# Performance work log

Hardware: AMD Instinct MI355X
Metric: run time of the kernel (lower is better)

The kernel has to match this reference:

```python
import jax, jax.numpy as jnp
import numpy as np

B, C, H, W = 4, 256, 64, 64
HID = C // 2


def setup_inputs() -> dict:
    key = jax.random.key(0)
    kx, kp, kt, kg, km = jax.random.split(key, 5)
    return {
        "x": jax.random.normal(kx, (B, C, H, W), dtype=jnp.float32),
        "w_phi": jax.random.normal(kp, (HID, C), dtype=jnp.float32) * 0.02,
        "w_theta": jax.random.normal(kt, (HID, C), dtype=jnp.float32) * 0.02,
        "w_g": jax.random.normal(kg, (HID, C), dtype=jnp.float32) * 0.02,
        "w_mask": jax.random.normal(km, (C, HID), dtype=jnp.float32) * 0.02,
    }


def reference(x, w_phi, w_theta, w_g, w_mask):
    b, c, h, w = x.shape
    n = h * w
    xf = x.reshape(b, c, n)                     # [B,C,N]
    # 1x1 convs == channel GEMMs
    phi = jnp.einsum('oc,bcn->bon', w_phi, xf)      # [B,HID,N]
    theta = jnp.einsum('oc,bcn->bon', w_theta, xf)  # [B,HID,N]
    g = jnp.einsum('oc,bcn->bon', w_g, xf)          # [B,HID,N]
    # attn[b,n,m] = sum_c theta[b,c,n] * phi[b,c,m]   (theta^T @ phi)
    attn = jnp.einsum('bcn,bcm->bnm', theta, phi)   # [B,N,N]
    # Faithful to nn.Softmax(dim=1): normalize over axis 1 (theta index)
    attn = jax.nn.softmax(attn, axis=1)
    # attn_g[b,n,c] = sum_m attn[b,n,m] * g[b,c,m]   (attn @ g^T)
    attn_g = jnp.einsum('bnm,bcm->bcn', attn, g)    # [B,HID,N] (already transposed back)
    mask = jnp.einsum('oc,bcn->bon', w_mask, attn_g).reshape(b, c, h, w)
    return mask + x
```

## Files before the change

### kernel.cpp

```cpp
#include <hip/hip_runtime.h>


#define NB   4
#define CIN  256
#define HIDN 128
#define NPIX 4096

typedef __attribute__((ext_vector_type(8))) short short8;
typedef __attribute__((ext_vector_type(4))) float f32x4;
typedef __attribute__((ext_vector_type(16))) float f32x16;

__device__ __forceinline__ unsigned short f2bf(float f) {
    unsigned u = __builtin_bit_cast(unsigned, f);
    u += 0x7fffu + ((u >> 16) & 1u);
    return (unsigned short)(u >> 16);
}
__device__ __forceinline__ unsigned f2bf2(float lo, float hi) {
    return (unsigned)f2bf(lo) | ((unsigned)f2bf(hi) << 16);
}
__device__ __forceinline__ unsigned pk2bf(float lo, float hi) {
#if __has_builtin(__builtin_amdgcn_cvt_pk_bf16_f32)
    typedef __attribute__((ext_vector_type(2))) __bf16 bf16x2;
    bf16x2 v = __builtin_amdgcn_cvt_pk_bf16_f32(lo, hi);
    return __builtin_bit_cast(unsigned, v);
#else
    return f2bf2(lo, hi);
#endif
}
__device__ __forceinline__ float fexp2(float x) {
#if __has_builtin(__builtin_amdgcn_exp2f)
    return __builtin_amdgcn_exp2f(x);
#else
    return exp2f(x);
#endif
}
__device__ __forceinline__ float bf2f(unsigned short s) {
    return __builtin_bit_cast(float, (unsigned)s << 16);
}
__device__ __forceinline__ void cp16(void* lds, const void* g) {
    __builtin_amdgcn_global_load_lds(
        (const __attribute__((address_space(1))) unsigned int*)g,
        (__attribute__((address_space(3))) unsigned int*)lds, 16, 0, 0);
}

__global__ __launch_bounds__(256) void k_prep_w(
    const float* __restrict__ wp, const float* __restrict__ wt,
    const float* __restrict__ wg, const float* __restrict__ wm,
    unsigned short* __restrict__ Wp, unsigned short* __restrict__ Wt,
    unsigned short* __restrict__ Wg, unsigned short* __restrict__ Wm)
{
    const int which = blockIdx.x >> 3;
    const float* src = (which == 0) ? wp : (which == 1) ? wt : (which == 2) ? wg : wm;
    unsigned short* dst = (which == 0) ? Wp : (which == 1) ? Wt : (which == 2) ? Wg : Wm;
#pragma unroll
    for (int t = 0; t < 2; ++t) {
        const int gidx = ((blockIdx.x & 7) * 256 + threadIdx.x) * 2 + t;
        int o, srcc, dstc;
        if (which < 3) {
            o = gidx >> 5;
            const int gc = gidx & 31;
            const int sg = (gc & ~15) | ((gc & 15) ^ (o & 15));
            srcc = o * 256 + gc * 8; dstc = o * 256 + sg * 8;
        } else {
            o = gidx >> 4;
            const int gc = gidx & 15;
            const int sg = gc ^ (o & 15);
            srcc = o * 128 + gc * 8; dstc = o * 128 + sg * 8;
        }
        float4 a = *(const float4*)&src[srcc];
        float4 b = *(const float4*)&src[srcc + 4];
        uint4 v;
        v.x = pk2bf(a.x, a.y); v.y = pk2bf(a.z, a.w);
        v.z = pk2bf(b.x, b.y); v.w = pk2bf(b.z, b.w);
        *(uint4*)&dst[dstc] = v;
    }
}

__global__ __launch_bounds__(256) void k_prep_x(
    const float* __restrict__ x,
    unsigned short* __restrict__ xT,
    float* __restrict__ colsum)
{
    const int nt = blockIdx.x, ct = blockIdx.y, b = blockIdx.z;
    const int tid = threadIdx.x;
    if (ct == 0 && tid < 64) colsum[(size_t)b * NPIX + nt * 64 + tid] = 0.f;

    __shared__ unsigned short Ls[64][66];
    {
        const int c_loc = tid >> 2, n_seg = (tid & 3) * 16;
        const float* src = x + ((size_t)(b * CIN + ct * 64 + c_loc)) * NPIX + nt * 64 + n_seg;
#pragma unroll
        for (int j = 0; j < 8; ++j)
            *(unsigned*)&Ls[c_loc][n_seg + 2 * j] = pk2bf(src[2 * j], src[2 * j + 1]);
    }
    __syncthreads();
    {
        const int n_loc = tid >> 2, c_seg = (tid & 3) * 16;
        const int n_glob = nt * 64 + n_loc;
        unsigned short tmp[16];
#pragma unroll
        for (int j = 0; j < 16; ++j) tmp[j] = Ls[c_seg + j][n_loc];
#pragma unroll
        for (int gr = 0; gr < 2; ++gr) {
            const int c_base = ct * 64 + c_seg + gr * 8;
            const int sec = c_base >> 7;
            const int sg = (((c_base >> 3) & 15) ^ (n_glob & 15));
            *(uint4*)&xT[((size_t)b * NPIX + n_glob) * CIN + sec * 128 + sg * 8] =
                *(uint4*)&tmp[gr * 8];
        }
    }
}

__global__ __launch_bounds__(256, 3) void k_proj(
    const unsigned short* __restrict__ Wp,
    const unsigned short* __restrict__ Wt,
    const unsigned short* __restrict__ Wg,
    const unsigned short* __restrict__ xT,
    unsigned short* __restrict__ phiT,
    unsigned short* __restrict__ thetaT,
    unsigned short* __restrict__ gbuf)
{
    const int nt = blockIdx.x, ot = blockIdx.y, b = blockIdx.z;
    const unsigned short* W = (ot == 0) ? Wp : (ot == 1) ? Wt : Wg;

    __shared__ alignas(16) unsigned short Aw[128][128];
    __shared__ alignas(16) unsigned short Bx[64][128];

    const int tid = threadIdx.x;
    const int wave = tid >> 6, lane = tid & 63;
    const int oh = wave >> 1, nh = wave & 1;
    const int l31 = lane & 31, lh = lane >> 5;
    const int key = l31 & 15;

    f32x16 acc[2];
#pragma unroll
    for (int r = 0; r < 16; ++r) { acc[0][r] = 0.f; acc[1][r] = 0.f; }

    for (int kh = 0; kh < 2; ++kh) {
        __syncthreads();
#pragma unroll
        for (int i = 0; i < 8; ++i) {
            const int u = i * 256 + tid;
            cp16(&Aw[0][0] + u * 8, W + (u >> 4) * 256 + kh * 128 + (u & 15) * 8);
        }
#pragma unroll
        for (int i = 0; i < 4; ++i) {
            const int u = i * 256 + tid;
            cp16(&Bx[0][0] + u * 8,
                 xT + ((size_t)b * NPIX + nt * 64 + (u >> 4)) * CIN + kh * 128 + (u & 15) * 8);
        }
        __syncthreads();
#pragma unroll
        for (int ks = 0; ks < 8; ++ks) {
            const int g = ((ks * 2 + lh) ^ key) << 3;
            short8 bb = *(const short8*)&Bx[nh * 32 + l31][g];
#pragma unroll
            for (int t = 0; t < 2; ++t) {
                short8 a = *(const short8*)&Aw[oh * 64 + t * 32 + l31][g];
                acc[t] = __builtin_amdgcn_mfma_f32_32x32x16_bf16(a, bb, acc[t], 0, 0, 0);
            }
        }
    }

    const int n_glob = nt * 64 + nh * 32 + l31;
    if (ot < 2) {
        unsigned short* T = (ot == 0) ? phiT : thetaT;
        const float osc = (ot == 1) ? 1.4426950408889634f : 1.0f;
#pragma unroll
        for (int t = 0; t < 2; ++t)
#pragma unroll
            for (int rg = 0; rg < 4; ++rg) {
                const int ob = oh * 64 + t * 32 + 8 * rg + 4 * lh;
                const int sc = (((ob >> 3) ^ (n_glob & 15)) << 3) | (ob & 7);
                uint2 v;
                v.x = pk2bf(acc[t][rg * 4 + 0] * osc, acc[t][rg * 4 + 1] * osc);
                v.y = pk2bf(acc[t][rg * 4 + 2] * osc, acc[t][rg * 4 + 3] * osc);
                *(uint2*)&T[((size_t)b * NPIX + n_glob) * HIDN + sc] = v;
            }
    } else {
        const int sbase = n_glob & ~127;
        const int g16 = (n_glob >> 3) & 15, c7off = n_glob & 7;
#pragma unroll
        for (int t = 0; t < 2; ++t)
#pragma unroll
            for (int r = 0; r < 16; ++r) {
                const int c = oh * 64 + t * 32 + (r & 3) + 8 * (r >> 2) + 4 * lh;
                const int sc = sbase | ((g16 ^ (c & 15)) << 3) | c7off;
                gbuf[((size_t)b * HIDN + c) * NPIX + sc] = f2bf(acc[t][r]);
            }
    }
}

__global__ __launch_bounds__(256, 3) void k_colsum(
    const unsigned short* __restrict__ thetaT,
    const unsigned short* __restrict__ phiT,
    float* __restrict__ colsum,
    float* __restrict__ O32)
{
    const int mt = blockIdx.x, ng = blockIdx.y, b = blockIdx.z;
    const int tid = threadIdx.x;
    {
        const int blin = ((blockIdx.z * 8 + blockIdx.y) * 32 + blockIdx.x);
        float* p = O32 + (size_t)blin * 2048 + tid * 8;
        *(f32x4*)p = f32x4{0.f, 0.f, 0.f, 0.f};
        *(f32x4*)(p + 4) = f32x4{0.f, 0.f, 0.f, 0.f};
    }

    __shared__ alignas(16) unsigned short As[2][64][128];

    const int wave = tid >> 6, lane = tid & 63;
    const int wn = wave & 1, wh = wave >> 1;
    const int l31 = lane & 31, lh = lane >> 5;
    const int key = l31 & 15;

    short8 bfrag[2][8];
#pragma unroll
    for (int t = 0; t < 2; ++t) {
        const int m = mt * 128 + wn * 64 + t * 32 + l31;
        const unsigned short* src = phiT + ((size_t)b * NPIX + m) * HIDN;
#pragma unroll
        for (int ks = 0; ks < 8; ++ks)
            bfrag[t][ks] = *(const short8*)(src + (((ks * 2 + lh) ^ key) << 3));
    }

#pragma unroll
    for (int i = 0; i < 4; ++i) {
        const int u = i * 256 + tid;
        cp16(&As[0][0][0] + u * 8,
             thetaT + ((size_t)b * NPIX + ng * 512 + (u >> 4)) * HIDN + (u & 15) * 8);
    }

    float csum[2] = {0.f, 0.f};

    for (int nc = 0; nc < 8; ++nc) {
        const int cur = nc & 1;
        __syncthreads();
        if (nc < 7) {
            const int n1 = ng * 512 + (nc + 1) * 64;
#pragma unroll
            for (int i = 0; i < 4; ++i) {
                const int u = i * 256 + tid;
                cp16(&As[cur ^ 1][0][0] + u * 8,
                     thetaT + ((size_t)b * NPIX + n1 + (u >> 4)) * HIDN + (u & 15) * 8);
            }
        }

        f32x16 acc[2];
#pragma unroll
        for (int r = 0; r < 16; ++r) { acc[0][r] = 0.f; acc[1][r] = 0.f; }
#pragma unroll
        for (int ks = 0; ks < 8; ++ks) {
            short8 a = *(const short8*)&As[cur][wh * 32 + l31][(((ks * 2 + lh) ^ key) << 3)];
            acc[0] = __builtin_amdgcn_mfma_f32_32x32x16_bf16(a, bfrag[0][ks], acc[0], 0, 0, 0);
            acc[1] = __builtin_amdgcn_mfma_f32_32x32x16_bf16(a, bfrag[1][ks], acc[1], 0, 0, 0);
        }
#pragma unroll
        for (int t = 0; t < 2; ++t)
#pragma unroll
            for (int r = 0; r < 16; ++r) csum[t] += fexp2(acc[t][r]);
    }

#pragma unroll
    for (int t = 0; t < 2; ++t) {
        float s = csum[t];
        s += __shfl_xor(s, 32);
        if (lh == 0)
            atomicAdd(&colsum[(size_t)b * NPIX + mt * 128 + wn * 64 + t * 32 + l31], s);
    }
}

__global__ __launch_bounds__(256) void k_scale_g(
    unsigned short* __restrict__ gbuf, const float* __restrict__ colsum)
{
    const int idx = blockIdx.x * 256 + threadIdx.x;
    const int row = idx >> 9;
    const int sc = (idx & 511) * 8;
    const int bb = row >> 7;
    const int mt = (sc & ~127) | ((((sc >> 3) & 15) ^ (row & 15)) << 3);
    uint4 v = *(uint4*)&gbuf[(size_t)row * NPIX + sc];
    float4 c0 = *(const float4*)&colsum[(size_t)bb * NPIX + mt];
    float4 c1 = *(const float4*)&colsum[(size_t)bb * NPIX + mt + 4];
    unsigned short* vs = (unsigned short*)&v;
    const float cs[8] = {c0.x, c0.y, c0.z, c0.w, c1.x, c1.y, c1.z, c1.w};
#pragma unroll
    for (int j = 0; j < 8; ++j) vs[j] = f2bf(bf2f(vs[j]) / cs[j]);
    *(uint4*)&gbuf[(size_t)row * NPIX + sc] = v;
}

__global__ __launch_bounds__(256, 2) void k_attn(
    const unsigned short* __restrict__ thetaT,
    const unsigned short* __restrict__ phiT,
    const unsigned short* __restrict__ gbuf,
    float* __restrict__ O32)
{
    const int nt = blockIdx.x, ms = blockIdx.y, b = blockIdx.z;
    const int n0 = nt * 64;

    __shared__ alignas(16) unsigned short Ps[2][64][128];

    const int tid = threadIdx.x;
    const int wave = tid >> 6, lane = tid & 63;
    const int q = wave;
    const int nh = wave >> 1, ch = wave & 1;
    const int l31 = lane & 31, lh = lane >> 5;
    const int key = l31 & 15;

    short8 tfrag[2][8];
#pragma unroll
    for (int t = 0; t < 2; ++t) {
        const unsigned short* src =
            thetaT + ((size_t)b * NPIX + n0 + t * 32 + l31) * HIDN;
#pragma unroll
        for (int ks = 0; ks < 8; ++ks)
            tfrag[t][ks] = *(const short8*)(src + (((ks * 2 + lh) ^ key) << 3));
    }

    const unsigned short* pphi =
        phiT + ((size_t)b * NPIX + ms * 2048 + q * 32 + l31) * HIDN;
    const unsigned short* pg0 =
        gbuf + ((size_t)b * HIDN + ch * 64 + l31) * NPIX + ms * 2048;
    const unsigned short* pg1 = pg0 + 32 * NPIX;

    f32x16 accO[2];
#pragma unroll
    for (int r = 0; r < 16; ++r) { accO[0][r] = 0.f; accO[1][r] = 0.f; }

    for (int mc = 0; mc < 16; ++mc) {
        const int cur = mc & 1;

        short8 pf[8], gf[2][8];
#pragma unroll
        for (int ks = 0; ks < 8; ++ks) {
            const int go = ((ks * 2 + lh) ^ key) << 3;
            pf[ks]    = *(const short8*)(pphi + go);
            gf[0][ks] = *(const short8*)(pg0 + go);
            gf[1][ks] = *(const short8*)(pg1 + go);
        }
        pphi += 128 * HIDN; pg0 += 128; pg1 += 128;

        f32x16 accS[2];
#pragma unroll
        for (int r = 0; r < 16; ++r) { accS[0][r] = 0.f; accS[1][r] = 0.f; }
#pragma unroll
        for (int ks = 0; ks < 8; ++ks) {
            accS[0] = __builtin_amdgcn_mfma_f32_32x32x16_bf16(pf[ks], tfrag[0][ks], accS[0], 0, 0, 0);
            accS[1] = __builtin_amdgcn_mfma_f32_32x32x16_bf16(pf[ks], tfrag[1][ks], accS[1], 0, 0, 0);
        }
#pragma unroll
        for (int t = 0; t < 2; ++t) {
            const int n = t * 32 + l31;
#pragma unroll
            for (int rg = 0; rg < 4; ++rg) {
                uint2 v;
                v.x = pk2bf(fexp2(accS[t][rg * 4 + 0]), fexp2(accS[t][rg * 4 + 1]));
                v.y = pk2bf(fexp2(accS[t][rg * 4 + 2]), fexp2(accS[t][rg * 4 + 3]));
                const int gm = q * 4 + rg;
                const int col = ((gm ^ (n & 15)) << 3) | (4 * lh);
                *(uint2*)&Ps[cur][n][col] = v;
            }
        }
        __syncthreads();

#pragma unroll
        for (int ks = 0; ks < 8; ++ks) {
            const int g = ((ks * 2 + lh) ^ key) << 3;
            short8 pa = *(const short8*)&Ps[cur][nh * 32 + l31][g];
            accO[0] = __builtin_amdgcn_mfma_f32_32x32x16_bf16(pa, gf[0][ks], accO[0], 0, 0, 0);
            accO[1] = __builtin_amdgcn_mfma_f32_32x32x16_bf16(pa, gf[1][ks], accO[1], 0, 0, 0);
        }
    }

#pragma unroll
    for (int t = 0; t < 2; ++t)
#pragma unroll
        for (int r = 0; r < 16; ++r) {
            const int n = n0 + nh * 32 + (r & 3) + 8 * (r >> 2) + 4 * lh;
            const int c = ch * 64 + t * 32 + l31;
            atomicAdd(&O32[((size_t)b * NPIX + n) * HIDN + c], accO[t][r]);
        }
}

__global__ __launch_bounds__(256, 3) void k_mask(
    const unsigned short* __restrict__ Wm,
    const float* __restrict__ O32,
    const float* __restrict__ x,
    float* __restrict__ out)
{
    const int nt = blockIdx.x, ct = blockIdx.y, b = blockIdx.z;
    __shared__ alignas(16) unsigned short As[128][128];
    __shared__ alignas(16) unsigned short Bs[64][128];

    const int tid = threadIdx.x;
    const int wave = tid >> 6, lane = tid & 63;
    const int oh = wave >> 1, nh = wave & 1;
    const int l31 = lane & 31, lh = lane >> 5;
    const int key = l31 & 15;

#pragma unroll
    for (int i = 0; i < 8; ++i) {
        const int u = i * 256 + tid;
        cp16(&As[0][0] + u * 8, Wm + (ct * 128 + (u >> 4)) * HIDN + (u & 15) * 8);
    }
    {
        const int n_loc = tid >> 2, seg = (tid & 3) * 32;
        const float* src = O32 + ((size_t)b * NPIX + nt * 64 + n_loc) * HIDN + seg;
        const int k7 = n_loc & 7;
#pragma unroll
        for (int j = 0; j < 4; ++j) {
            const int gr = (seg >> 3) + j;
            const int sg = (gr & ~7) | ((gr & 7) ^ k7);
            const float* s8 = src + j * 8;
            unsigned* d = (unsigned*)&Bs[n_loc][sg * 8];
#pragma unroll
            for (int k = 0; k < 4; ++k) d[k] = pk2bf(s8[2 * k], s8[2 * k + 1]);
        }
    }
    __syncthreads();

    f32x16 acc[2];
#pragma unroll
    for (int r = 0; r < 16; ++r) { acc[0][r] = 0.f; acc[1][r] = 0.f; }
#pragma unroll
    for (int ks = 0; ks < 8; ++ks) {
        const int gr = ks * 2 + lh;
        const int sgb = ((gr & ~7) | ((gr & 7) ^ (l31 & 7))) << 3;
        short8 bb = *(const short8*)&Bs[nh * 32 + l31][sgb];
#pragma unroll
        for (int t = 0; t < 2; ++t) {
            short8 a = *(const short8*)&As[oh * 64 + t * 32 + l31][((gr ^ key) << 3)];
            acc[t] = __builtin_amdgcn_mfma_f32_32x32x16_bf16(a, bb, acc[t], 0, 0, 0);
        }
    }

    const int n = nt * 64 + nh * 32 + l31;
#pragma unroll
    for (int t = 0; t < 2; ++t)
#pragma unroll
        for (int r = 0; r < 16; ++r) {
            const int co = ct * 128 + oh * 64 + t * 32 + (r & 3) + 8 * (r >> 2) + 4 * lh;
            const size_t idx = ((size_t)b * CIN + co) * NPIX + n;
            out[idx] = acc[t][r] + x[idx];
        }
}

extern "C" void kernel_launch(void* const* d_in, const int* in_sizes, int n_in,
                              void* d_out, int out_size, void* d_ws, size_t ws_size,
                              hipStream_t stream)
{
    (void)in_sizes; (void)n_in; (void)out_size; (void)ws_size;
    const float* x       = (const float*)d_in[0];
    const float* w_phi   = (const float*)d_in[1];
    const float* w_theta = (const float*)d_in[2];
    const float* w_g     = (const float*)d_in[3];
    const float* w_mask  = (const float*)d_in[4];
    float* out = (float*)d_out;

    char* ws = (char*)d_ws;
    unsigned short* phiT   = (unsigned short*)(ws);
    unsigned short* thetaT = (unsigned short*)(ws + 4194304);
    unsigned short* gbuf   = (unsigned short*)(ws + 8388608);
    float*          colsum = (float*)(ws + 12582912);
    unsigned short* xT     = (unsigned short*)(ws + 12648448);
    float*          O32    = (float*)(ws + 12648448);
    unsigned short* Wp     = (unsigned short*)(ws + 21037056);
    unsigned short* Wt     = (unsigned short*)(ws + 21102592);
    unsigned short* Wg     = (unsigned short*)(ws + 21168128);
    unsigned short* Wm     = (unsigned short*)(ws + 21233664);

    k_prep_w <<<dim3(32),        256, 0, stream>>>(w_phi, w_theta, w_g, w_mask, Wp, Wt, Wg, Wm);
    k_prep_x <<<dim3(64, 4, 4),  256, 0, stream>>>(x, xT, colsum);
    k_proj   <<<dim3(64, 3, 4),  256, 0, stream>>>(Wp, Wt, Wg, xT, phiT, thetaT, gbuf);
    k_colsum <<<dim3(32, 8, 4),  256, 0, stream>>>(thetaT, phiT, colsum, O32);
    k_scale_g<<<dim3(1024),      256, 0, stream>>>(gbuf, colsum);
    k_attn   <<<dim3(64, 2, 4),  256, 0, stream>>>(thetaT, phiT, gbuf, O32);
    k_mask   <<<dim3(64, 2, 4),  256, 0, stream>>>(Wm, O32, x, out);
}
```

Before: 187.1 us.

## Stage g tiles through LDS with async double-buffering and prefetch phi

The attention kernel now loads each g tile cooperatively into a double-buffered LDS array with cp16 async copies, issued for the next chunk while the current chunk's PV MFMAs run. Phi fragments are register double-buffered so the next chunk's loads overlap the current QK MFMAs. The P buffer drops to a single copy, and a second barrier per iteration protects it. This aims to hide global load latency and cut redundant per-wave g loads, at the cost of more LDS (about 80KB per block), which may limit occupancy to fewer than the two blocks per CU requested.

```diff
diff --git a/kernel.cpp b/kernel.cpp
--- a/kernel.cpp
+++ b/kernel.cpp
@@ -296,7 +296,8 @@
     const int nt = blockIdx.x, ms = blockIdx.y, b = blockIdx.z;
     const int n0 = nt * 64;
 
-    __shared__ alignas(16) unsigned short Ps[2][64][128];
+    __shared__ alignas(16) unsigned short Gs[2][128][128];
+    __shared__ alignas(16) unsigned short Ps[64][128];
 
     const int tid = threadIdx.x;
     const int wave = tid >> 6, lane = tid & 63;
@@ -314,12 +315,20 @@
         for (int ks = 0; ks < 8; ++ks)
             tfrag[t][ks] = *(const short8*)(src + (((ks * 2 + lh) ^ key) << 3));
     }
-
+    short8 pf[2][8];
     const unsigned short* pphi =
         phiT + ((size_t)b * NPIX + ms * 2048 + q * 32 + l31) * HIDN;
-    const unsigned short* pg0 =
-        gbuf + ((size_t)b * HIDN + ch * 64 + l31) * NPIX + ms * 2048;
-    const unsigned short* pg1 = pg0 + 32 * NPIX;
+#pragma unroll
+    for (int ks = 0; ks < 8; ++ks)
+        pf[0][ks] = *(const short8*)(pphi + (((ks * 2 + lh) ^ key) << 3));
+    pphi += 128 * HIDN;
+
+#pragma unroll
+    for (int i = 0; i < 8; ++i) {
+        const int u = i * 256 + tid;
+        cp16(&Gs[0][0][0] + u * 8,
+             gbuf + ((size_t)b * HIDN + (u >> 4)) * NPIX + ms * 2048 + (u & 15) * 8);
+    }
 
     f32x16 accO[2];
 #pragma unroll
@@ -327,24 +336,21 @@
 
     for (int mc = 0; mc < 16; ++mc) {
         const int cur = mc & 1;
-
-        short8 pf[8], gf[2][8];
+        const int m0 = ms * 2048 + mc * 128;
+
+        f32x16 accS[2];
+#pragma unroll
+        for (int r = 0; r < 16; ++r) { accS[0][r] = 0.f; accS[1][r] = 0.f; }
 #pragma unroll
         for (int ks = 0; ks < 8; ++ks) {
-            const int go = ((ks * 2 + lh) ^ key) << 3;
-            pf[ks]    = *(const short8*)(pphi + go);
-            gf[0][ks] = *(const short8*)(pg0 + go);
-            gf[1][ks] = *(const short8*)(pg1 + go);
-        }
-        pphi += 128 * HIDN; pg0 += 128; pg1 += 128;
-
-        f32x16 accS[2];
-#pragma unroll
-        for (int r = 0; r < 16; ++r) { accS[0][r] = 0.f; accS[1][r] = 0.f; }
-#pragma unroll
-        for (int ks = 0; ks < 8; ++ks) {
-            accS[0] = __builtin_amdgcn_mfma_f32_32x32x16_bf16(pf[ks], tfrag[0][ks], accS[0], 0, 0, 0);
-            accS[1] = __builtin_amdgcn_mfma_f32_32x32x16_bf16(pf[ks], tfrag[1][ks], accS[1], 0, 0, 0);
+            accS[0] = __builtin_amdgcn_mfma_f32_32x32x16_bf16(pf[cur][ks], tfrag[0][ks], accS[0], 0, 0, 0);
+            accS[1] = __builtin_amdgcn_mfma_f32_32x32x16_bf16(pf[cur][ks], tfrag[1][ks], accS[1], 0, 0, 0);
+        }
+        if (mc < 15) {
+#pragma unroll
+            for (int ks = 0; ks < 8; ++ks)
+                pf[cur ^ 1][ks] = *(const short8*)(pphi + (((ks * 2 + lh) ^ key) << 3));
+            pphi += 128 * HIDN;
         }
 #pragma unroll
         for (int t = 0; t < 2; ++t) {
@@ -356,18 +362,28 @@
                 v.y = pk2bf(fexp2(accS[t][rg * 4 + 2]), fexp2(accS[t][rg * 4 + 3]));
                 const int gm = q * 4 + rg;
                 const int col = ((gm ^ (n & 15)) << 3) | (4 * lh);
-                *(uint2*)&Ps[cur][n][col] = v;
+                *(uint2*)&Ps[n][col] = v;
             }
         }
         __syncthreads();
-
+        if (mc < 15) {
+#pragma unroll
+            for (int i = 0; i < 8; ++i) {
+                const int u = i * 256 + tid;
+                cp16(&Gs[cur ^ 1][0][0] + u * 8,
+                     gbuf + ((size_t)b * HIDN + (u >> 4)) * NPIX + m0 + 128 + (u & 15) * 8);
+            }
+        }
 #pragma unroll
         for (int ks = 0; ks < 8; ++ks) {
             const int g = ((ks * 2 + lh) ^ key) << 3;
-            short8 pa = *(const short8*)&Ps[cur][nh * 32 + l31][g];
-            accO[0] = __builtin_amdgcn_mfma_f32_32x32x16_bf16(pa, gf[0][ks], accO[0], 0, 0, 0);
-            accO[1] = __builtin_amdgcn_mfma_f32_32x32x16_bf16(pa, gf[1][ks], accO[1], 0, 0, 0);
-        }
+            short8 pa = *(const short8*)&Ps[nh * 32 + l31][g];
+            short8 g0 = *(const short8*)&Gs[cur][ch * 64 + l31][g];
+            short8 g1 = *(const short8*)&Gs[cur][ch * 64 + 32 + l31][g];
+            accO[0] = __builtin_amdgcn_mfma_f32_32x32x16_bf16(pa, g0, accO[0], 0, 0, 0);
+            accO[1] = __builtin_amdgcn_mfma_f32_32x32x16_bf16(pa, g1, accO[1], 0, 0, 0);
+        }
+        __syncthreads();
     }
 
 #pragma unroll
```

New measurement: 230.3 us. 1.23x slower.
